# Kernel tuning notes

Measured on AMD Instinct MI355X. Metric: run time of the kernel, lower is better.

## Reference

```python
import jax, jax.numpy as jnp
import numpy as np

EPS = 1e-08
TEMPERATURE = 1.0
HEADS = 4
OUT_DIM = 32
IN_DIM = 128
N_NODES = 100000
N_EDGES = 1600000


def setup_inputs() -> dict:
    key = jax.random.key(0)
    k1, k2, k3, k4, k5, k6 = jax.random.split(key, 6)
    x = jax.random.normal(k1, (N_NODES, IN_DIM), dtype=jnp.float32)
    # nn.Linear(in_dim, heads*out_dim, bias=False).weight -> [heads*out_dim, in_dim]
    W = jax.random.normal(k2, (HEADS * OUT_DIM, IN_DIM), dtype=jnp.float32) * 0.05
    a_src = jax.random.normal(k3, (HEADS, OUT_DIM), dtype=jnp.float32) * 0.1
    a_dst = jax.random.normal(k4, (HEADS, OUT_DIM), dtype=jnp.float32) * 0.1
    edge_index = jax.random.randint(k5, (2, N_EDGES), 0, N_NODES, dtype=jnp.int32)
    rnbrw_weights = jax.random.uniform(k6, (N_EDGES,), dtype=jnp.float32)
    return {"x": x, "W": W, "a_src": a_src, "a_dst": a_dst,
            "edge_index": edge_index, "rnbrw_weights": rnbrw_weights}


def reference(x, W, a_src, a_dst, edge_index, rnbrw_weights):
    N = x.shape[0]
    heads, out_dim = a_src.shape
    # h = W(x).view(N, heads, out_dim)
    h = (x @ W.T).reshape(N, heads, out_dim)
    src, dst = edge_index[0], edge_index[1]
    h_src = h[src]  # [E, heads, out_dim]
    h_dst = h[dst]  # [E, heads, out_dim]
    # per-edge attention scores [E, heads]
    score = jnp.einsum('ehd,hd->eh', h_src, a_src) + jnp.einsum('ehd,hd->eh', h_dst, a_dst)
    # strategy == 'pre_softmax_bias'
    score = score + jnp.log(rnbrw_weights + EPS)[:, None]
    score = jnp.where(score >= 0, score, 0.2 * score)  # leaky_relu(0.2)
    scaled = score / TEMPERATURE
    # edge softmax over incoming edges of each dst node
    seg_max = jax.ops.segment_max(scaled, dst, num_segments=N)      # [N, heads]
    exp_s = jnp.exp(scaled - seg_max[dst])                           # [E, heads]
    denom = jax.ops.segment_sum(exp_s, dst, num_segments=N)         # [N, heads]
    alpha = exp_s / (denom[dst] + EPS)                               # [E, heads]
    # scatter-add aggregation: out[dst] += alpha * h_src
    out = jax.ops.segment_sum(alpha[..., None] * h_src, dst, num_segments=N)
    out = out.reshape(N, heads * out_dim)
    return out, alpha
```

## Files before the change

kernel.cpp:

```cpp
#include <hip/hip_runtime.h>

#define EPS 1e-8f

__device__ inline unsigned short f2bf(float f) {
    unsigned u = __float_as_uint(f);
    unsigned r = u + 0x7fffu + ((u >> 16) & 1u);
    return (unsigned short)(r >> 16);
}
__device__ inline float bflo(unsigned v) { return __uint_as_float(v << 16); }
__device__ inline float bfhi(unsigned v) { return __uint_as_float(v & 0xffff0000u); }

__device__ inline float bsel(float4 es4, int i, int head) {
    float x = __shfl(es4.x, i, 32);
    float y = __shfl(es4.y, i, 32);
    float z = __shfl(es4.z, i, 32);
    float w = __shfl(es4.w, i, 32);
    return head == 0 ? x : head == 1 ? y : head == 2 ? z : w;
}

__global__ __launch_bounds__(256) void gemm_s_kernel(
    const float* __restrict__ x, const float* __restrict__ W,
    const float* __restrict__ a_src, const float* __restrict__ a_dst,
    unsigned short* __restrict__ hb, float* __restrict__ s_src, float* __restrict__ s_dst,
    int N, int n_tiles)
{
    __shared__ float Wt[128 * 64];
    __shared__ float xt[128 * 64];

    const int t = threadIdx.x;
    const int half = blockIdx.y;
    const float* Wh = W + half * 64 * 128;

#pragma unroll
    for (int p = 0; p < 8; ++p) {
        int idx = p * 256 + t;
        int ol = (idx & 31) | ((idx >> 10) << 5);
        int k4 = (idx >> 5) & 31;
        float4 w = *(const float4*)(Wh + ol * 128 + k4 * 4);
        Wt[(4 * k4 + 0) * 64 + ol] = w.x;
        Wt[(4 * k4 + 1) * 64 + ol] = w.y;
        Wt[(4 * k4 + 2) * 64 + ol] = w.z;
        Wt[(4 * k4 + 3) * 64 + ol] = w.w;
    }
    __syncthreads();

    const int o4 = t & 15;
    const int n4g = t >> 4;
    const int head = half * 2 + (o4 >> 3);
    const float4 as = *(const float4*)(a_src + head * 32 + (o4 & 7) * 4);
    const float4 ad = *(const float4*)(a_dst + head * 32 + (o4 & 7) * 4);

    for (int tile = blockIdx.x; tile < n_tiles; tile += gridDim.x) {
        const int nbase = tile * 64;
        __syncthreads();
#pragma unroll
        for (int p = 0; p < 8; ++p) {
            int idx = p * 256 + t;
            int n = idx & 63;
            int k4 = idx >> 6;
            int ng = nbase + n;
            float4 v = make_float4(0.f, 0.f, 0.f, 0.f);
            if (ng < N) v = *(const float4*)(x + (size_t)ng * 128 + k4 * 4);
            xt[(4 * k4 + 0) * 64 + n] = v.x;
            xt[(4 * k4 + 1) * 64 + n] = v.y;
            xt[(4 * k4 + 2) * 64 + n] = v.z;
            xt[(4 * k4 + 3) * 64 + n] = v.w;
        }
        __syncthreads();

        float acc[4][4];
#pragma unroll
        for (int i = 0; i < 4; ++i)
#pragma unroll
            for (int j = 0; j < 4; ++j) acc[i][j] = 0.f;

        for (int k = 0; k < 128; ++k) {
            float4 wv = *(const float4*)(Wt + k * 64 + 4 * o4);
            float4 xv = *(const float4*)(xt + k * 64 + 4 * n4g);
            float wa[4] = {wv.x, wv.y, wv.z, wv.w};
            float xa[4] = {xv.x, xv.y, xv.z, xv.w};
#pragma unroll
            for (int i = 0; i < 4; ++i)
#pragma unroll
                for (int j = 0; j < 4; ++j) acc[i][j] += xa[i] * wa[j];
        }

#pragma unroll
        for (int i = 0; i < 4; ++i) {
            int n = nbase + 4 * n4g + i;
            float ps = acc[i][0] * as.x + acc[i][1] * as.y + acc[i][2] * as.z + acc[i][3] * as.w;
            float pd = acc[i][0] * ad.x + acc[i][1] * ad.y + acc[i][2] * ad.z + acc[i][3] * ad.w;
            ps += __shfl_xor(ps, 1); ps += __shfl_xor(ps, 2); ps += __shfl_xor(ps, 4);
            pd += __shfl_xor(pd, 1); pd += __shfl_xor(pd, 2); pd += __shfl_xor(pd, 4);
            if (n < N) {
                ushort4 hv;
                hv.x = f2bf(acc[i][0]); hv.y = f2bf(acc[i][1]);
                hv.z = f2bf(acc[i][2]); hv.w = f2bf(acc[i][3]);
                *(ushort4*)(hb + (size_t)n * 128 + half * 64 + 4 * o4) = hv;
                if ((o4 & 7) == 0) {
                    s_src[n * 4 + head] = ps;
                    s_dst[n * 4 + head] = pd;
                }
            }
        }
    }
}

__global__ __launch_bounds__(256) void edge_score_kernel(
    const int* __restrict__ src, const int* __restrict__ dst,
    const float* __restrict__ rnbrw,
    const float* __restrict__ s_src, const float* __restrict__ s_dst,
    float* __restrict__ es_orig, int* __restrict__ counts, int E)
{
    int e = blockIdx.x * 256 + threadIdx.x;
    if (e >= E) return;
    int s = src[e], d = dst[e];
    float lw = __logf(rnbrw[e] + EPS);
    float4 a = *(const float4*)(s_src + s * 4);
    float4 b = *(const float4*)(s_dst + d * 4);
    float sc[4] = {a.x + b.x + lw, a.y + b.y + lw, a.z + b.z + lw, a.w + b.w + lw};
    float es[4];
#pragma unroll
    for (int hh = 0; hh < 4; ++hh) {
        float v = sc[hh];
        v = (v >= 0.f) ? v : 0.2f * v;
        es[hh] = __expf(v);
    }
    *(float4*)(es_orig + (size_t)e * 4) = make_float4(es[0], es[1], es[2], es[3]);
    atomicAdd(counts + d, 1);
}

__global__ __launch_bounds__(256) void scan1_kernel(
    const int* __restrict__ counts, int* __restrict__ offs, int* __restrict__ bsum, int N)
{
    __shared__ int sh[256];
    int t = threadIdx.x;
    int base = blockIdx.x * 1024 + t * 4;
    int c[4];
#pragma unroll
    for (int j = 0; j < 4; ++j) c[j] = (base + j < N) ? counts[base + j] : 0;
    int tsum = c[0] + c[1] + c[2] + c[3];
    sh[t] = tsum;
    __syncthreads();
    for (int off = 1; off < 256; off <<= 1) {
        int v = (t >= off) ? sh[t - off] : 0;
        __syncthreads();
        sh[t] += v;
        __syncthreads();
    }
    int run = sh[t] - tsum;
    if (t == 255) bsum[blockIdx.x] = sh[255];
#pragma unroll
    for (int j = 0; j < 4; ++j) {
        if (base + j < N) { offs[base + j] = run; run += c[j]; }
    }
}

__global__ void scan2_kernel(int* __restrict__ bsum, int nb)
{
    if (threadIdx.x == 0) {
        int acc = 0;
        for (int i = 0; i < nb; ++i) { int v = bsum[i]; bsum[i] = acc; acc += v; }
    }
}

__global__ __launch_bounds__(256) void scan3_kernel(
    int* __restrict__ offs, const int* __restrict__ bsum,
    int* __restrict__ cursor, int N)
{
    int i = blockIdx.x * 256 + threadIdx.x;
    if (i >= N) return;
    int v = offs[i] + bsum[i >> 10];
    offs[i] = v;
    cursor[i] = v;
}

__global__ __launch_bounds__(256) void scatter_kernel(
    const int* __restrict__ src, const int* __restrict__ dst,
    const float* __restrict__ es_orig, int* __restrict__ cursor,
    int* __restrict__ csr_src, int* __restrict__ csr_eid,
    float* __restrict__ csr_es, int E)
{
    int e = blockIdx.x * 256 + threadIdx.x;
    if (e >= E) return;
    int pos = atomicAdd(cursor + dst[e], 1);
    csr_src[pos] = src[e];
    csr_eid[pos] = e;
    *(float4*)(csr_es + (size_t)pos * 4) = *(const float4*)(es_orig + (size_t)e * 4);
}

__global__ __launch_bounds__(256) void node_aggr_kernel(
    const int* __restrict__ offs, const int* __restrict__ counts,
    const int* __restrict__ csr_src, const int* __restrict__ csr_eid,
    const float* __restrict__ csr_es,
    const unsigned short* __restrict__ hb,
    float* __restrict__ alpha, float* __restrict__ out, int N)
{
    int gid = blockIdx.x * 256 + threadIdx.x;
    int n = gid >> 5;
    int l = gid & 31;
    if (n >= N) return;

    int beg = offs[n];
    int cnt = counts[n];
    int head = l >> 3;

    float4 acc = make_float4(0.f, 0.f, 0.f, 0.f);
    float den = 0.f;

    for (int base = 0; base < cnt; base += 32) {
        int m = cnt - base; if (m > 32) m = 32;
        int sl = 0;
        float4 es4 = make_float4(0.f, 0.f, 0.f, 0.f);
        if (l < m) {
            int p = beg + base + l;
            sl = csr_src[p];
            es4 = *(const float4*)(csr_es + (size_t)p * 4);
        }
        int mr = (m + 3) & ~3;
        for (int i = 0; i < mr; i += 4) {
            int s0 = __shfl(sl, i + 0, 32);
            int s1 = __shfl(sl, i + 1, 32);
            int s2 = __shfl(sl, i + 2, 32);
            int s3 = __shfl(sl, i + 3, 32);
            uint2 v0 = *(const uint2*)(hb + (size_t)s0 * 128 + l * 4);
            uint2 v1 = *(const uint2*)(hb + (size_t)s1 * 128 + l * 4);
            uint2 v2 = *(const uint2*)(hb + (size_t)s2 * 128 + l * 4);
            uint2 v3 = *(const uint2*)(hb + (size_t)s3 * 128 + l * 4);
            float e0 = bsel(es4, i + 0, head);
            float e1 = bsel(es4, i + 1, head);
            float e2 = bsel(es4, i + 2, head);
            float e3 = bsel(es4, i + 3, head);
            acc.x += e0 * bflo(v0.x); acc.y += e0 * bfhi(v0.x);
            acc.z += e0 * bflo(v0.y); acc.w += e0 * bfhi(v0.y);
            acc.x += e1 * bflo(v1.x); acc.y += e1 * bfhi(v1.x);
            acc.z += e1 * bflo(v1.y); acc.w += e1 * bfhi(v1.y);
            acc.x += e2 * bflo(v2.x); acc.y += e2 * bfhi(v2.x);
            acc.z += e2 * bflo(v2.y); acc.w += e2 * bfhi(v2.y);
            acc.x += e3 * bflo(v3.x); acc.y += e3 * bfhi(v3.x);
            acc.z += e3 * bflo(v3.y); acc.w += e3 * bfhi(v3.y);
            den += e0 + e1 + e2 + e3;
        }
    }

    float inv_h[4];
#pragma unroll
    for (int q = 0; q < 4; ++q) {
        float dq = __shfl(den, q << 3, 32);
        inv_h[q] = 1.f / (dq + EPS);
    }

    float inv = inv_h[head];
    acc.x *= inv; acc.y *= inv; acc.z *= inv; acc.w *= inv;
    *(float4*)(out + (size_t)n * 128 + l * 4) = acc;

    for (int base = 0; base < cnt; base += 32) {
        int m = cnt - base; if (m > 32) m = 32;
        if (l < m) {
            int p = beg + base + l;
            int eid = csr_eid[p];
            float4 es4 = *(const float4*)(csr_es + (size_t)p * 4);
            float4 al = make_float4(es4.x * inv_h[0], es4.y * inv_h[1],
                                    es4.z * inv_h[2], es4.w * inv_h[3]);
            *(float4*)(alpha + (size_t)eid * 4) = al;
        }
    }
}

extern "C" void kernel_launch(void* const* d_in, const int* in_sizes, int n_in,
                              void* d_out, int out_size, void* d_ws, size_t ws_size,
                              hipStream_t stream) {
    const float* x      = (const float*)d_in[0];
    const float* W      = (const float*)d_in[1];
    const float* a_src  = (const float*)d_in[2];
    const float* a_dst  = (const float*)d_in[3];
    const int*   eidx   = (const int*)d_in[4];
    const float* rnbrw  = (const float*)d_in[5];

    const int E = in_sizes[5];
    const int N = in_sizes[0] / 128;

    float* out   = (float*)d_out;
    float* alpha = out + (size_t)N * 128;
    float* es_orig = alpha;

    char* w = (char*)d_ws;
    unsigned short* hb = (unsigned short*)w;  w += (size_t)N * 128 * 2;
    float* s_src = (float*)w;                 w += (size_t)N * 4 * 4;
    float* s_dst = (float*)w;                 w += (size_t)N * 4 * 4;
    int* counts  = (int*)w;                   w += (size_t)N * 4;
    int* offs    = (int*)w;                   w += (size_t)N * 4;
    int* cursor  = (int*)w;                   w += (size_t)N * 4;
    int* bsum    = (int*)w;                   w += 512;
    int* csr_src = (int*)w;                   w += (size_t)E * 4;
    int* csr_eid = (int*)w;                   w += (size_t)E * 4;
    float* csr_es = (float*)w;

    const int* src = eidx;
    const int* dst = eidx + E;

    hipMemsetAsync(counts, 0, (size_t)N * sizeof(int), stream);

    int n_tiles = (N + 63) / 64;
    dim3 gridA(512, 2);
    gemm_s_kernel<<<gridA, 256, 0, stream>>>(x, W, a_src, a_dst, hb, s_src, s_dst, N, n_tiles);

    int eblocks = (E + 255) / 256;
    edge_score_kernel<<<eblocks, 256, 0, stream>>>(src, dst, rnbrw, s_src, s_dst,
                                                   es_orig, counts, E);

    int nb = (N + 1023) / 1024;
    scan1_kernel<<<nb, 256, 0, stream>>>(counts, offs, bsum, N);
    scan2_kernel<<<1, 64, 0, stream>>>(bsum, nb);
    scan3_kernel<<<(N + 255) / 256, 256, 0, stream>>>(offs, bsum, cursor, N);

    scatter_kernel<<<eblocks, 256, 0, stream>>>(src, dst, es_orig, cursor,
                                                csr_src, csr_eid, csr_es, E);

    int ablocks = ((size_t)N * 32 + 255) / 256;
    node_aggr_kernel<<<ablocks, 256, 0, stream>>>(offs, counts, csr_src, csr_eid,
                                                  csr_es, hb, alpha, out, N);
}
```

Baseline: 442.9 us.

## Recompute edge scores on the fly instead of materializing per-edge exp buffers

Result: slower. 483.1 us (+9.1%).

```diff
diff --git a/kernel.cpp b/kernel.cpp
--- a/kernel.cpp
+++ b/kernel.cpp
@@ -9,6 +9,11 @@
 }
 __device__ inline float bflo(unsigned v) { return __uint_as_float(v << 16); }
 __device__ inline float bfhi(unsigned v) { return __uint_as_float(v & 0xffff0000u); }
+
+__device__ inline float leaky_exp(float v) {
+    v = (v >= 0.f) ? v : 0.2f * v;
+    return __expf(v);
+}
 
 __device__ inline float bsel(float4 es4, int i, int head) {
     float x = __shfl(es4.x, i, 32);
@@ -106,28 +111,11 @@
     }
 }
 
-__global__ __launch_bounds__(256) void edge_score_kernel(
-    const int* __restrict__ src, const int* __restrict__ dst,
-    const float* __restrict__ rnbrw,
-    const float* __restrict__ s_src, const float* __restrict__ s_dst,
-    float* __restrict__ es_orig, int* __restrict__ counts, int E)
+__global__ __launch_bounds__(256) void hist_kernel(
+    const int* __restrict__ dst, int* __restrict__ counts, int E)
 {
     int e = blockIdx.x * 256 + threadIdx.x;
-    if (e >= E) return;
-    int s = src[e], d = dst[e];
-    float lw = __logf(rnbrw[e] + EPS);
-    float4 a = *(const float4*)(s_src + s * 4);
-    float4 b = *(const float4*)(s_dst + d * 4);
-    float sc[4] = {a.x + b.x + lw, a.y + b.y + lw, a.z + b.z + lw, a.w + b.w + lw};
-    float es[4];
-#pragma unroll
-    for (int hh = 0; hh < 4; ++hh) {
-        float v = sc[hh];
-        v = (v >= 0.f) ? v : 0.2f * v;
-        es[hh] = __expf(v);
-    }
-    *(float4*)(es_orig + (size_t)e * 4) = make_float4(es[0], es[1], es[2], es[3]);
-    atomicAdd(counts + d, 1);
+    if (e < E) atomicAdd(counts + dst[e], 1);
 }
 
 __global__ __launch_bounds__(256) void scan1_kernel(
@@ -177,24 +165,22 @@
 
 __global__ __launch_bounds__(256) void scatter_kernel(
     const int* __restrict__ src, const int* __restrict__ dst,
-    const float* __restrict__ es_orig, int* __restrict__ cursor,
-    int* __restrict__ csr_src, int* __restrict__ csr_eid,
-    float* __restrict__ csr_es, int E)
+    const float* __restrict__ rnbrw, int* __restrict__ cursor,
+    int2* __restrict__ recs, int E)
 {
     int e = blockIdx.x * 256 + threadIdx.x;
     if (e >= E) return;
+    float lw = __logf(rnbrw[e] + EPS);
     int pos = atomicAdd(cursor + dst[e], 1);
-    csr_src[pos] = src[e];
-    csr_eid[pos] = e;
-    *(float4*)(csr_es + (size_t)pos * 4) = *(const float4*)(es_orig + (size_t)e * 4);
+    recs[pos] = make_int2(src[e], __float_as_int(lw));
 }
 
 __global__ __launch_bounds__(256) void node_aggr_kernel(
     const int* __restrict__ offs, const int* __restrict__ counts,
-    const int* __restrict__ csr_src, const int* __restrict__ csr_eid,
-    const float* __restrict__ csr_es,
+    const int2* __restrict__ recs, const float* __restrict__ s_src,
+    const float* __restrict__ s_dst,
     const unsigned short* __restrict__ hb,
-    float* __restrict__ alpha, float* __restrict__ out, int N)
+    float* __restrict__ inv_tab, float* __restrict__ out, int N)
 {
     int gid = blockIdx.x * 256 + threadIdx.x;
     int n = gid >> 5;
@@ -204,6 +190,8 @@
     int beg = offs[n];
     int cnt = counts[n];
     int head = l >> 3;
+
+    const float4 sd = *(const float4*)(s_dst + (size_t)n * 4);
 
     float4 acc = make_float4(0.f, 0.f, 0.f, 0.f);
     float den = 0.f;
@@ -213,9 +201,14 @@
         int sl = 0;
         float4 es4 = make_float4(0.f, 0.f, 0.f, 0.f);
         if (l < m) {
-            int p = beg + base + l;
-            sl = csr_src[p];
-            es4 = *(const float4*)(csr_es + (size_t)p * 4);
+            int2 rec = recs[beg + base + l];
+            sl = rec.x;
+            float lw = __int_as_float(rec.y);
+            float4 ss = *(const float4*)(s_src + (size_t)sl * 4);
+            es4.x = leaky_exp(ss.x + sd.x + lw);
+            es4.y = leaky_exp(ss.y + sd.y + lw);
+            es4.z = leaky_exp(ss.z + sd.z + lw);
+            es4.w = leaky_exp(ss.w + sd.w + lw);
         }
         int mr = (m + 3) & ~3;
         for (int i = 0; i < mr; i += 4) {
@@ -254,17 +247,30 @@
     acc.x *= inv; acc.y *= inv; acc.z *= inv; acc.w *= inv;
     *(float4*)(out + (size_t)n * 128 + l * 4) = acc;
 
-    for (int base = 0; base < cnt; base += 32) {
-        int m = cnt - base; if (m > 32) m = 32;
-        if (l < m) {
-            int p = beg + base + l;
-            int eid = csr_eid[p];
-            float4 es4 = *(const float4*)(csr_es + (size_t)p * 4);
-            float4 al = make_float4(es4.x * inv_h[0], es4.y * inv_h[1],
-                                    es4.z * inv_h[2], es4.w * inv_h[3]);
-            *(float4*)(alpha + (size_t)eid * 4) = al;
-        }
-    }
+    if (l == 0)
+        *(float4*)(inv_tab + (size_t)n * 4) =
+            make_float4(inv_h[0], inv_h[1], inv_h[2], inv_h[3]);
+}
+
+__global__ __launch_bounds__(256) void alpha_kernel(
+    const int* __restrict__ src, const int* __restrict__ dst,
+    const float* __restrict__ rnbrw,
+    const float* __restrict__ s_src, const float* __restrict__ s_dst,
+    const float* __restrict__ inv_tab, float* __restrict__ alpha, int E)
+{
+    int e = blockIdx.x * 256 + threadIdx.x;
+    if (e >= E) return;
+    int s = src[e], d = dst[e];
+    float lw = __logf(rnbrw[e] + EPS);
+    float4 a = *(const float4*)(s_src + (size_t)s * 4);
+    float4 b = *(const float4*)(s_dst + (size_t)d * 4);
+    float4 iv = *(const float4*)(inv_tab + (size_t)d * 4);
+    float4 al;
+    al.x = leaky_exp(a.x + b.x + lw) * iv.x;
+    al.y = leaky_exp(a.y + b.y + lw) * iv.y;
+    al.z = leaky_exp(a.z + b.z + lw) * iv.z;
+    al.w = leaky_exp(a.w + b.w + lw) * iv.w;
+    *(float4*)(alpha + (size_t)e * 4) = al;
 }
 
 extern "C" void kernel_launch(void* const* d_in, const int* in_sizes, int n_in,
@@ -282,19 +288,17 @@
 
     float* out   = (float*)d_out;
     float* alpha = out + (size_t)N * 128;
-    float* es_orig = alpha;
 
     char* w = (char*)d_ws;
     unsigned short* hb = (unsigned short*)w;  w += (size_t)N * 128 * 2;
-    float* s_src = (float*)w;                 w += (size_t)N * 4 * 4;
-    float* s_dst = (float*)w;                 w += (size_t)N * 4 * 4;
-    int* counts  = (int*)w;                   w += (size_t)N * 4;
-    int* offs    = (int*)w;                   w += (size_t)N * 4;
-    int* cursor  = (int*)w;                   w += (size_t)N * 4;
-    int* bsum    = (int*)w;                   w += 512;
-    int* csr_src = (int*)w;                   w += (size_t)E * 4;
-    int* csr_eid = (int*)w;                   w += (size_t)E * 4;
-    float* csr_es = (float*)w;
+    float* s_src  = (float*)w;                w += (size_t)N * 4 * 4;
+    float* s_dst  = (float*)w;                w += (size_t)N * 4 * 4;
+    float* inv_tab= (float*)w;                w += (size_t)N * 4 * 4;
+    int* counts   = (int*)w;                  w += (size_t)N * 4;
+    int* offs     = (int*)w;                  w += (size_t)N * 4;
+    int* cursor   = (int*)w;                  w += (size_t)N * 4;
+    int* bsum     = (int*)w;                  w += 512;
+    int2* recs    = (int2*)w;
 
     const int* src = eidx;
     const int* dst = eidx + E;
@@ -306,18 +310,19 @@
     gemm_s_kernel<<<gridA, 256, 0, stream>>>(x, W, a_src, a_dst, hb, s_src, s_dst, N, n_tiles);
 
     int eblocks = (E + 255) / 256;
-    edge_score_kernel<<<eblocks, 256, 0, stream>>>(src, dst, rnbrw, s_src, s_dst,
-                                                   es_orig, counts, E);
+    hist_kernel<<<eblocks, 256, 0, stream>>>(dst, counts, E);
 
     int nb = (N + 1023) / 1024;
     scan1_kernel<<<nb, 256, 0, stream>>>(counts, offs, bsum, N);
     scan2_kernel<<<1, 64, 0, stream>>>(bsum, nb);
     scan3_kernel<<<(N + 255) / 256, 256, 0, stream>>>(offs, bsum, cursor, N);
 
-    scatter_kernel<<<eblocks, 256, 0, stream>>>(src, dst, es_orig, cursor,
-                                                csr_src, csr_eid, csr_es, E);
+    scatter_kernel<<<eblocks, 256, 0, stream>>>(src, dst, rnbrw, cursor, recs, E);
 
     int ablocks = ((size_t)N * 32 + 255) / 256;
-    node_aggr_kernel<<<ablocks, 256, 0, stream>>>(offs, counts, csr_src, csr_eid,
-                                                  csr_es, hb, alpha, out, N);
-}
+    node_aggr_kernel<<<ablocks, 256, 0, stream>>>(offs, counts, recs, s_src, s_dst,
+                                                  hb, inv_tab, out, N);
+
+    alpha_kernel<<<eblocks, 256, 0, stream>>>(src, dst, rnbrw, s_src, s_dst,
+                                              inv_tab, alpha, E);
+}
```
